# Kernel optimization log

Hardware: AMD Instinct MI355X
Metric: run time of the kernel (lower is better)

Reference implementation:

```python
import jax, jax.numpy as jnp
import numpy as np

N_AGENTS, RNN_H, N_HEADS, GAT_D, EMB, SDIM = 16, 64, 4, 32, 32, 128


def setup_inputs() -> dict:
    key = jax.random.key(0)
    ks = jax.random.split(key, 16)
    xav = lambda k, shp: jax.random.normal(k, shp, jnp.float32) * (2.0 / sum(shp)) ** 0.5
    return {
        'agent_qs': jax.random.normal(ks[0], (32, 128, N_AGENTS), jnp.float32),
        'states': jax.random.normal(ks[1], (32, 128, SDIM), jnp.float32),
        'hidden_states': jax.random.normal(ks[2], (32, 128, N_AGENTS, RNN_H), jnp.float32),
        'uncertainty': jax.random.uniform(ks[3], (32, 128, 1), jnp.float32),
        'W_gat': xav(ks[4], (RNN_H, N_HEADS * GAT_D)) * 1.414,
        'att_a': xav(ks[5], (1, N_HEADS, 2 * GAT_D)) * 1.414,
        'w1s_W': xav(ks[6], (SDIM + 1, N_HEADS * EMB * GAT_D)),
        'w1s_b': jnp.zeros((N_HEADS * EMB * GAT_D,), jnp.float32),
        'b1_W': xav(ks[7], (SDIM, EMB)),
        'b1_b': jnp.zeros((EMB,), jnp.float32),
        'wf_W': xav(ks[8], (SDIM, EMB)),
        'wf_b': jnp.zeros((EMB,), jnp.float32),
        'V1_W': xav(ks[9], (SDIM, EMB)),
        'V1_b': jnp.zeros((EMB,), jnp.float32),
        'V2_W': xav(ks[10], (EMB, 1)),
        'V2_b': jnp.zeros((1,), jnp.float32),
    }


def gat(h, W_gat, att_a):
    B, n, _ = h.shape
    hp = (h @ W_gat).reshape(B, n, N_HEADS, GAT_D).transpose(0, 2, 1, 3)  # (B,H,n,d)
    a_src, a_dst = att_a[0, :, :GAT_D], att_a[0, :, GAT_D:]  # (H,d) each
    # e[b,h,i,j] = <hp_i, a_src> + <hp_j, a_dst>  (same math as concat+dot)
    src = jnp.einsum('bhnd,hd->bhn', hp, a_src)
    dst = jnp.einsum('bhnd,hd->bhn', hp, a_dst)
    e = jax.nn.leaky_relu(src[:, :, :, None] + dst[:, :, None, :], 0.2)
    attn = jax.nn.softmax(e, axis=-1)
    return jax.nn.elu(jnp.einsum('bhij,bhjd->bhid', attn, hp))  # (B,H,n,d)


def reference(agent_qs, states, hidden_states, uncertainty, W_gat, att_a,
              w1s_W, w1s_b, b1_W, b1_b, wf_W, wf_b, V1_W, V1_b, V2_W, V2_b):
    bs = agent_qs.shape[0]
    s = states.reshape(-1, SDIM)                      # (B,S)
    qs = agent_qs.reshape(-1, 1, N_AGENTS)            # (B,1,n)
    hs = hidden_states.reshape(-1, N_AGENTS, RNN_H)   # (B,n,R)
    unc = uncertainty.reshape(-1, 1)
    s_aug = jnp.concatenate([s, unc], axis=1)         # (B,S+1)

    g = gat(hs, W_gat, att_a)                         # (B,H,n,d)

    w1_state = (s_aug @ w1s_W + w1s_b).reshape(-1, N_HEADS, EMB, GAT_D)
    w1_heads = jnp.abs(jnp.einsum('bhed,bhnd->bhen', w1_state, g))  # (B,H,E,n)
    w1 = w1_heads.mean(axis=1).transpose(0, 2, 1)     # (B,n,E)

    b1 = (s @ b1_W + b1_b)[:, None, :]                # (B,1,E)
    hidden = jax.nn.elu(jnp.einsum('bin,bne->bie', qs, w1) + b1)  # (B,1,E)

    w_final = jnp.abs(s @ wf_W + wf_b)[:, :, None]    # (B,E,1)
    v = (jax.nn.relu(s @ V1_W + V1_b) @ V2_W + V2_b)[:, None, :]  # (B,1,1)
    y = jnp.einsum('bie,bej->bij', hidden, w_final) + v
    return y.reshape(bs, -1, 1)
```

## Files before the change

### kernel.cpp

```cpp
#include <hip/hip_runtime.h>
#include <hip/hip_bf16.h>
#include <math.h>


typedef __attribute__((ext_vector_type(8))) short short8;
typedef __attribute__((ext_vector_type(8))) unsigned short ushort8;
typedef __attribute__((ext_vector_type(4))) float float4v;
typedef __attribute__((ext_vector_type(4))) _Float16 half4v;

static __device__ inline unsigned short f2bf(float f) {
    unsigned int x;
    __builtin_memcpy(&x, &f, 4);
    unsigned int r = x + 0x7fffu + ((x >> 16) & 1u);
    return (unsigned short)(r >> 16);
}

static __device__ inline unsigned int cvtpk(float lo, float hi) {
    __hip_bfloat162 h = __float22bfloat162_rn(make_float2(lo, hi));
    unsigned int u;
    __builtin_memcpy(&u, &h, 4);
    return u;
}

static __device__ inline short8 pack8(float4 f0, float4 f1) {
    unsigned int u[4] = {cvtpk(f0.x, f0.y), cvtpk(f0.z, f0.w),
                         cvtpk(f1.x, f1.y), cvtpk(f1.z, f1.w)};
    short8 s;
    __builtin_memcpy(&s, u, 16);
    return s;
}

__global__ __launch_bounds__(256) void k0_prep(
    const float* __restrict__ w1s_W,
    const float* __restrict__ W_gat,
    const float* __restrict__ att_a,
    const float* __restrict__ states,
    const float* __restrict__ b1_W, const float* __restrict__ b1_b,
    const float* __restrict__ wf_W, const float* __restrict__ wf_b,
    const float* __restrict__ V1_W, const float* __restrict__ V1_b,
    const float* __restrict__ V2_W, const float* __restrict__ V2_b,
    unsigned short* __restrict__ w1sTf,
    unsigned short* __restrict__ WgTf,
    unsigned short* __restrict__ Sbf,
    float* __restrict__ b1v, float* __restrict__ wfv,
    float* __restrict__ out)
{
    __shared__ __align__(16) char SMEM[26112];
    const int tid = threadIdx.x, bx = blockIdx.x;

    if (bx < 256) {
        unsigned short* T = (unsigned short*)SMEM;
        const int c0 = bx * 16;
        const int cc = tid & 15, kr = tid >> 4;
        #pragma unroll
        for (int t = 0; t < 8; ++t) {
            int k = t * 16 + kr;
            T[cc * 136 + k] = f2bf(w1s_W[(size_t)k * 4096 + c0 + cc]);
        }
        __syncthreads();
        const int ks = tid >> 6, q = (tid >> 4) & 3, mm = tid & 15;
        *(ushort8*)&w1sTf[(size_t)bx * 2048 + tid * 8] =
            *(const ushort8*)&T[mm * 136 + ks * 32 + q * 8];
    } else if (bx == 256) {
        unsigned short* T = (unsigned short*)SMEM;
        #pragma unroll
        for (int t = 0; t < 32; ++t) {
            int i = t * 256 + tid;
            int k = i >> 7, c = i & 127;
            T[c * 72 + k] = f2bf(W_gat[k * 128 + c]);
        }
        __syncthreads();
        #pragma unroll
        for (int t = 0; t < 4; ++t) {
            int i = t * 256 + tid;
            int nt = i >> 7, w = i & 127;
            int kh = w >> 6, q = (w >> 4) & 3, mm = w & 15;
            *(ushort8*)&WgTf[nt * 1024 + w * 8] =
                *(const ushort8*)&T[(nt * 16 + mm) * 72 + kh * 32 + q * 8];
        }
        {
            const int k = tid >> 2, h = tid & 3;
            float ss = 0.f, dd = 0.f;
            #pragma unroll
            for (int d = 0; d < 32; ++d) {
                float wv = W_gat[k * 128 + h * 32 + d];
                ss = fmaf(wv, att_a[h * 64 + d], ss);
                dd = fmaf(wv, att_a[h * 64 + 32 + d], dd);
            }
            const int base = 8192 + (k >> 5) * 512 + ((k >> 3) & 3) * 128 + (k & 7);
            WgTf[base + h * 8]       = f2bf(ss);
            WgTf[base + (4 + h) * 8] = f2bf(dd);
        }
        #pragma unroll
        for (int t = 0; t < 2; ++t) {
            int i = t * 256 + tid;
            int kh = i >> 8, q = (i >> 6) & 3, mm = 8 + ((i >> 3) & 7), j = i & 7;
            WgTf[8192 + kh * 512 + q * 128 + mm * 8 + j] = 0;
        }
    } else {
        unsigned short* WLu = (unsigned short*)SMEM;
        for (int i = tid; i < 12288; i += 256) {
            float v = (i < 4096) ? b1_W[i] : (i < 8192 ? wf_W[i - 4096] : V1_W[i - 8192]);
            int set = i >> 12, k = (i >> 5) & 127, e = i & 31;
            WLu[set * 4352 + k * 34 + e] = f2bf(v);
        }
        __syncthreads();

        const int wave = tid >> 6, lane = tid & 63, mm = lane & 15, q = lane >> 4;
        const int b0w = (bx - 257) * 64 + wave * 16;

        short8 a[4];
        #pragma unroll
        for (int ks = 0; ks < 4; ++ks) {
            const float* sp = states + (size_t)(b0w + mm) * 128 + ks * 32 + q * 8;
            a[ks] = pack8(*(const float4*)sp, *(const float4*)(sp + 4));
        }
        #pragma unroll
        for (int ks = 0; ks < 4; ++ks)
            *(short8*)&Sbf[(size_t)(b0w + mm) * 128 + ks * 32 + q * 8] = a[ks];

        float4v accT[6];
        #pragma unroll
        for (int nt = 0; nt < 6; ++nt) accT[nt] = (float4v){0.f, 0.f, 0.f, 0.f};
        #pragma unroll
        for (int nt = 0; nt < 6; ++nt) {
            const int set = nt >> 1, e = (nt & 1) * 16 + mm;
            #pragma unroll
            for (int ks = 0; ks < 4; ++ks) {
                ushort8 bfu;
                #pragma unroll
                for (int j = 0; j < 8; ++j)
                    bfu[j] = WLu[set * 4352 + (ks * 32 + q * 8 + j) * 34 + e];
                short8 bf;
                __builtin_memcpy(&bf, &bfu, 16);
                accT[nt] = __builtin_amdgcn_mfma_f32_16x16x32_bf16(a[ks], bf, accT[nt], 0, 0, 0);
            }
        }
        float vsum[4] = {0.f, 0.f, 0.f, 0.f};
        #pragma unroll
        for (int p = 0; p < 2; ++p) {
            const int e = p * 16 + mm;
            const float bb1 = b1_b[e], bwf = wf_b[e], bv1 = V1_b[e], v2 = V2_W[e];
            #pragma unroll
            for (int reg = 0; reg < 4; ++reg) {
                const int row = b0w + q * 4 + reg;
                b1v[(size_t)row * 32 + e] = accT[p][reg] + bb1;
                wfv[(size_t)row * 32 + e] = fabsf(accT[2 + p][reg] + bwf);
                vsum[reg] += fmaxf(accT[4 + p][reg] + bv1, 0.f) * v2;
            }
        }
        #pragma unroll
        for (int reg = 0; reg < 4; ++reg) {
            vsum[reg] += __shfl_xor(vsum[reg], 1);
            vsum[reg] += __shfl_xor(vsum[reg], 2);
            vsum[reg] += __shfl_xor(vsum[reg], 4);
            vsum[reg] += __shfl_xor(vsum[reg], 8);
        }
        if (mm == 0) {
            #pragma unroll
            for (int reg = 0; reg < 4; ++reg)
                out[b0w + q * 4 + reg] = vsum[reg] + V2_b[0];
        }
    }
}

__global__ __launch_bounds__(256) void k2a_gemm(
    const unsigned short* __restrict__ w1sTf,
    const unsigned short* __restrict__ Sbf,
    const float* __restrict__ uncertainty,
    const float* __restrict__ w1s_W,
    const float* __restrict__ w1s_b,
    unsigned short* __restrict__ W2)
{
    const int bx = blockIdx.x;
    const int rb = bx >> 4, pg = bx & 15;
    const int wave = threadIdx.x >> 6, lane = threadIdx.x & 63;
    const int m = lane & 15, quad = lane >> 4;
    const int ep = pg * 4 + wave;
    const int ct0 = ep * 4;

    const float* w128 = w1s_W + (size_t)128 * 4096;

    short8 A[4][4];
    #pragma unroll
    for (int t = 0; t < 4; ++t)
        #pragma unroll
        for (int ks = 0; ks < 4; ++ks)
            A[t][ks] = *(const short8*)&w1sTf[(size_t)(ct0 + t) * 2048 + ks * 512 + lane * 8];

    float wf[4][4], bb[4][4];
    #pragma unroll
    for (int t = 0; t < 4; ++t) {
        float4 w4 = *(const float4*)&w128[(ct0 + t) * 16 + quad * 4];
        float4 b4 = *(const float4*)&w1s_b[(ct0 + t) * 16 + quad * 4];
        wf[t][0] = w4.x; wf[t][1] = w4.y; wf[t][2] = w4.z; wf[t][3] = w4.w;
        bb[t][0] = b4.x; bb[t][1] = b4.y; bb[t][2] = b4.z; bb[t][3] = b4.w;
    }

    #pragma unroll
    for (int c = 0; c < 4; ++c) {
        const int r0c = rb * 64 + c * 16;
        const float us = uncertainty[r0c + m];
        short8 Bf[4];
        #pragma unroll
        for (int ks = 0; ks < 4; ++ks)
            Bf[ks] = *(const short8*)&Sbf[(size_t)(r0c + m) * 128 + ks * 32 + quad * 8];

        float4v z[4];
        #pragma unroll
        for (int t = 0; t < 4; ++t) z[t] = (float4v){0.f, 0.f, 0.f, 0.f};
        #pragma unroll
        for (int t = 0; t < 4; ++t)
            #pragma unroll
            for (int ks = 0; ks < 4; ++ks)
                z[t] = __builtin_amdgcn_mfma_f32_16x16x32_bf16(A[t][ks], Bf[ks], z[t], 0, 0, 0);

        #pragma unroll
        for (int half = 0; half < 2; ++half) {
            const int tA = half * 2, tB = half * 2 + 1;
            unsigned int wpk[4];
            #pragma unroll
            for (int reg = 0; reg < 4; ++reg) {
                float za = z[tA][reg] + us * wf[tA][reg] + bb[tA][reg];
                float zb = z[tB][reg] + us * wf[tB][reg] + bb[tB][reg];
                wpk[reg] = cvtpk(za, zb);
            }
            short8 pk;
            __builtin_memcpy(&pk, wpk, 16);
            const int E = ep * 2 + half;
            const int eo = (E >> 4) * 512 + (E & 15) * 32 + quad * 8;
            *(short8*)&W2[(size_t)(r0c + m) * 4096 + eo] = pk;
        }
    }
}

__global__ __launch_bounds__(256) void k1_gatmix(
    const float* __restrict__ hidden_states,
    const unsigned short* __restrict__ WgTf,
    const unsigned short* __restrict__ W2,
    const float* __restrict__ agent_qs,
    const float* __restrict__ b1v, const float* __restrict__ wfv,
    float* __restrict__ out)
{
    const int wave = threadIdx.x >> 6;
    const int b = blockIdx.x * 4 + wave;
    const int lane = threadIdx.x & 63, m = lane & 15, quad = lane >> 4;
    __shared__ __align__(16) float sc[4 * 320];
    float* scr = &sc[wave * 320];

    short8 wfr[8];
    #pragma unroll
    for (int i = 0; i < 8; ++i)
        wfr[i] = *(const short8*)&W2[(size_t)b * 4096 + i * 512 + m * 32 + quad * 8];
    const float qs_m = agent_qs[b * 16 + m];

    const float* hrow = hidden_states + ((size_t)b * 16 + m) * 64;
    float4 f0 = *(const float4*)(hrow + quad * 8);
    float4 f1 = *(const float4*)(hrow + quad * 8 + 4);
    short8 a0 = pack8(f0, f1);
    f0 = *(const float4*)(hrow + 32 + quad * 8);
    f1 = *(const float4*)(hrow + 32 + quad * 8 + 4);
    short8 a1 = pack8(f0, f1);

    float4v hpt[9];
    #pragma unroll
    for (int nt = 0; nt < 9; ++nt) {
        short8 bf0 = *(const short8*)&WgTf[nt * 1024 + lane * 8];
        short8 bf1 = *(const short8*)&WgTf[nt * 1024 + 512 + lane * 8];
        float4v z = (float4v){0.f, 0.f, 0.f, 0.f};
        z = __builtin_amdgcn_mfma_f32_16x16x32_bf16(a0, bf0, z, 0, 0, 0);
        z = __builtin_amdgcn_mfma_f32_16x16x32_bf16(a1, bf1, z, 0, 0, 0);
        hpt[nt] = z;
    }

    {
        float4 pr = {hpt[8][0], hpt[8][1], hpt[8][2], hpt[8][3]};
        *(float4*)&scr[m * 20 + quad * 4] = pr;
    }

    float Sacc[2][4] = {};

    #pragma unroll
    for (int h = 0; h < 4; ++h) {
        const float src_m = scr[h * 20 + m];
        float4 pdv = *(const float4*)&scr[(4 + h) * 20 + quad * 4];
        float pd[4] = {pdv.x, pdv.y, pdv.z, pdv.w};

        float e_[4];
        #pragma unroll
        for (int jj = 0; jj < 4; ++jj) {
            float x = src_m + pd[jj];
            e_[jj] = fmaxf(x, 0.2f * x);
        }
        float mx = fmaxf(fmaxf(e_[0], e_[1]), fmaxf(e_[2], e_[3]));
        mx = fmaxf(mx, __shfl_xor(mx, 16));
        mx = fmaxf(mx, __shfl_xor(mx, 32));
        float p_[4], ssum = 0.f;
        #pragma unroll
        for (int jj = 0; jj < 4; ++jj) { p_[jj] = __expf(e_[jj] - mx); ssum += p_[jj]; }
        ssum += __shfl_xor(ssum, 16);
        ssum += __shfl_xor(ssum, 32);
        const float inv = __builtin_amdgcn_rcpf(ssum);

        half4v bfrag;
        #pragma unroll
        for (int jj = 0; jj < 4; ++jj) bfrag[jj] = (_Float16)(p_[jj] * inv);

        float4v zp[2];
        #pragma unroll
        for (int p = 0; p < 2; ++p) {
            float4v ct = hpt[2 * h + p];
            half4v afrag;
            #pragma unroll
            for (int t = 0; t < 4; ++t) afrag[t] = (_Float16)ct[t];
            float4v z = (float4v){0.f, 0.f, 0.f, 0.f};
            zp[p] = __builtin_amdgcn_mfma_f32_16x16x16f16(afrag, bfrag, z, 0, 0, 0);
        }
        unsigned int w[4];
        #pragma unroll
        for (int t = 0; t < 4; ++t) {
            float x0 = zp[0][t];
            x0 = (x0 > 0.f) ? x0 : (__expf(x0) - 1.f);
            float x1 = zp[1][t];
            x1 = (x1 > 0.f) ? x1 : (__expf(x1) - 1.f);
            w[t] = cvtpk(x0, x1);
        }
        short8 gfrag;
        __builtin_memcpy(&gfrag, w, 16);

        #pragma unroll
        for (int H = 0; H < 2; ++H) {
            float4v z = (float4v){0.f, 0.f, 0.f, 0.f};
            z = __builtin_amdgcn_mfma_f32_16x16x32_bf16(wfr[h * 2 + H], gfrag, z, 0, 0, 0);
            #pragma unroll
            for (int reg = 0; reg < 4; ++reg)
                Sacc[H][reg] += fabsf(z[reg]);
        }
    }

    float local = 0.f;
    #pragma unroll
    for (int H = 0; H < 2; ++H) {
        float sn[4];
        #pragma unroll
        for (int reg = 0; reg < 4; ++reg) sn[reg] = Sacc[H][reg] * qs_m;
        #pragma unroll
        for (int mask = 1; mask <= 8; mask <<= 1) {
            #pragma unroll
            for (int reg = 0; reg < 4; ++reg) sn[reg] += __shfl_xor(sn[reg], mask);
        }
        float4 b4 = *(const float4*)&b1v[(size_t)b * 32 + H * 16 + quad * 4];
        float4 w4 = *(const float4*)&wfv[(size_t)b * 32 + H * 16 + quad * 4];
        float bq[4] = {b4.x, b4.y, b4.z, b4.w};
        float wq[4] = {w4.x, w4.y, w4.z, w4.w};
        #pragma unroll
        for (int reg = 0; reg < 4; ++reg) {
            float hid = 0.25f * sn[reg] + bq[reg];
            hid = (hid > 0.f) ? hid : expm1f(hid);
            local = fmaf(hid, wq[reg], local);
        }
    }
    local += __shfl_xor(local, 16);
    local += __shfl_xor(local, 32);
    if (lane == 0) out[b] = out[b] + local;
}

extern "C" void kernel_launch(void* const* d_in, const int* in_sizes, int n_in,
                              void* d_out, int out_size, void* d_ws, size_t ws_size,
                              hipStream_t stream)
{
    const float* agent_qs      = (const float*)d_in[0];
    const float* states        = (const float*)d_in[1];
    const float* hidden_states = (const float*)d_in[2];
    const float* uncertainty   = (const float*)d_in[3];
    const float* W_gat         = (const float*)d_in[4];
    const float* att_a         = (const float*)d_in[5];
    const float* w1s_W         = (const float*)d_in[6];
    const float* w1s_b         = (const float*)d_in[7];
    const float* b1_W          = (const float*)d_in[8];
    const float* b1_b          = (const float*)d_in[9];
    const float* wf_W          = (const float*)d_in[10];
    const float* wf_b          = (const float*)d_in[11];
    const float* V1_W          = (const float*)d_in[12];
    const float* V1_b          = (const float*)d_in[13];
    const float* V2_W          = (const float*)d_in[14];
    const float* V2_b          = (const float*)d_in[15];

    char* w = (char*)d_ws;
    unsigned short* w1sTf   = (unsigned short*)w;  w += (size_t)524288 * 2;
    unsigned short* WgTf    = (unsigned short*)w;  w += (size_t)9216 * 2;
    unsigned short* Sbf     = (unsigned short*)w;  w += (size_t)524288 * 2;
    unsigned short* W2      = (unsigned short*)w;  w += (size_t)16777216 * 2;
    float* b1v              = (float*)w;           w += (size_t)131072 * 4;
    float* wfv              = (float*)w;           w += (size_t)131072 * 4;
    float* out              = (float*)d_out;

    k0_prep<<<321, 256, 0, stream>>>(w1s_W, W_gat, att_a, states,
                                     b1_W, b1_b, wf_W, wf_b, V1_W, V1_b,
                                     V2_W, V2_b, w1sTf, WgTf, Sbf, b1v, wfv, out);

    k2a_gemm<<<1024, 256, 0, stream>>>(w1sTf, Sbf, uncertainty, w1s_W, w1s_b, W2);

    k1_gatmix<<<1024, 256, 0, stream>>>(hidden_states, WgTf, W2, agent_qs,
                                        b1v, wfv, out);
}
```

Before: 130.3 us.

## Split GAT-mix work per head across waves and halve GEMM tile per wave

The GAT mixing kernel now assigns one batch element per block, with each of the four waves handling one attention head, and combines head results through shared memory after a block barrier. The W2 GEMM kernel gives each wave one embedding pair instead of two, doubling its grid. The aim is more parallelism and fewer live registers per wave, which should raise occupancy. In exchange, each block of the mixing kernel recomputes the shared projection tile and adds a __syncthreads plus shared-memory reduction, and both kernels now launch more blocks.

```diff
diff --git a/kernel.cpp b/kernel.cpp
--- a/kernel.cpp
+++ b/kernel.cpp
@@ -173,30 +173,32 @@
     unsigned short* __restrict__ W2)
 {
     const int bx = blockIdx.x;
-    const int rb = bx >> 4, pg = bx & 15;
+    const int rb = bx >> 5, pg = bx & 31;
     const int wave = threadIdx.x >> 6, lane = threadIdx.x & 63;
     const int m = lane & 15, quad = lane >> 4;
-    const int ep = pg * 4 + wave;
-    const int ct0 = ep * 4;
+    const int E = pg * 4 + wave;
+    const int ct0 = E * 2;
 
     const float* w128 = w1s_W + (size_t)128 * 4096;
 
-    short8 A[4][4];
-    #pragma unroll
-    for (int t = 0; t < 4; ++t)
+    short8 A[2][4];
+    #pragma unroll
+    for (int t = 0; t < 2; ++t)
         #pragma unroll
         for (int ks = 0; ks < 4; ++ks)
             A[t][ks] = *(const short8*)&w1sTf[(size_t)(ct0 + t) * 2048 + ks * 512 + lane * 8];
 
-    float wf[4][4], bb[4][4];
-    #pragma unroll
-    for (int t = 0; t < 4; ++t) {
+    float wf[2][4], bb[2][4];
+    #pragma unroll
+    for (int t = 0; t < 2; ++t) {
         float4 w4 = *(const float4*)&w128[(ct0 + t) * 16 + quad * 4];
         float4 b4 = *(const float4*)&w1s_b[(ct0 + t) * 16 + quad * 4];
         wf[t][0] = w4.x; wf[t][1] = w4.y; wf[t][2] = w4.z; wf[t][3] = w4.w;
         bb[t][0] = b4.x; bb[t][1] = b4.y; bb[t][2] = b4.z; bb[t][3] = b4.w;
     }
 
+    const int eo = (E >> 4) * 512 + (E & 15) * 32 + quad * 8;
+
     #pragma unroll
     for (int c = 0; c < 4; ++c) {
         const int r0c = rb * 64 + c * 16;
@@ -206,31 +208,23 @@
         for (int ks = 0; ks < 4; ++ks)
             Bf[ks] = *(const short8*)&Sbf[(size_t)(r0c + m) * 128 + ks * 32 + quad * 8];
 
-        float4v z[4];
-        #pragma unroll
-        for (int t = 0; t < 4; ++t) z[t] = (float4v){0.f, 0.f, 0.f, 0.f};
-        #pragma unroll
-        for (int t = 0; t < 4; ++t)
-            #pragma unroll
-            for (int ks = 0; ks < 4; ++ks)
-                z[t] = __builtin_amdgcn_mfma_f32_16x16x32_bf16(A[t][ks], Bf[ks], z[t], 0, 0, 0);
-
-        #pragma unroll
-        for (int half = 0; half < 2; ++half) {
-            const int tA = half * 2, tB = half * 2 + 1;
-            unsigned int wpk[4];
-            #pragma unroll
-            for (int reg = 0; reg < 4; ++reg) {
-                float za = z[tA][reg] + us * wf[tA][reg] + bb[tA][reg];
-                float zb = z[tB][reg] + us * wf[tB][reg] + bb[tB][reg];
-                wpk[reg] = cvtpk(za, zb);
-            }
-            short8 pk;
-            __builtin_memcpy(&pk, wpk, 16);
-            const int E = ep * 2 + half;
-            const int eo = (E >> 4) * 512 + (E & 15) * 32 + quad * 8;
-            *(short8*)&W2[(size_t)(r0c + m) * 4096 + eo] = pk;
-        }
+        float4v z0 = (float4v){0.f, 0.f, 0.f, 0.f};
+        float4v z1 = (float4v){0.f, 0.f, 0.f, 0.f};
+        #pragma unroll
+        for (int ks = 0; ks < 4; ++ks) {
+            z0 = __builtin_amdgcn_mfma_f32_16x16x32_bf16(A[0][ks], Bf[ks], z0, 0, 0, 0);
+            z1 = __builtin_amdgcn_mfma_f32_16x16x32_bf16(A[1][ks], Bf[ks], z1, 0, 0, 0);
+        }
+        unsigned int wpk[4];
+        #pragma unroll
+        for (int reg = 0; reg < 4; ++reg) {
+            float za = z0[reg] + us * wf[0][reg] + bb[0][reg];
+            float zb = z1[reg] + us * wf[1][reg] + bb[1][reg];
+            wpk[reg] = cvtpk(za, zb);
+        }
+        short8 pk;
+        __builtin_memcpy(&pk, wpk, 16);
+        *(short8*)&W2[(size_t)(r0c + m) * 4096 + eo] = pk;
     }
 }
 
@@ -242,16 +236,17 @@
     const float* __restrict__ b1v, const float* __restrict__ wfv,
     float* __restrict__ out)
 {
-    const int wave = threadIdx.x >> 6;
-    const int b = blockIdx.x * 4 + wave;
+    const int h = threadIdx.x >> 6;
+    const int b = blockIdx.x;
     const int lane = threadIdx.x & 63, m = lane & 15, quad = lane >> 4;
     __shared__ __align__(16) float sc[4 * 320];
-    float* scr = &sc[wave * 320];
-
-    short8 wfr[8];
-    #pragma unroll
-    for (int i = 0; i < 8; ++i)
-        wfr[i] = *(const short8*)&W2[(size_t)b * 4096 + i * 512 + m * 32 + quad * 8];
+    __shared__ float red[128];
+    float* scr = &sc[h * 320];
+
+    short8 wfr[2];
+    #pragma unroll
+    for (int H = 0; H < 2; ++H)
+        wfr[H] = *(const short8*)&W2[(size_t)b * 4096 + (h * 2 + H) * 512 + m * 32 + quad * 8];
     const float qs_m = agent_qs[b * 16 + m];
 
     const float* hrow = hidden_states + ((size_t)b * 16 + m) * 64;
@@ -262,107 +257,110 @@
     f1 = *(const float4*)(hrow + 32 + quad * 8 + 4);
     short8 a1 = pack8(f0, f1);
 
-    float4v hpt[9];
-    #pragma unroll
-    for (int nt = 0; nt < 9; ++nt) {
+    float4v hpt[2], prj;
+    #pragma unroll
+    for (int p = 0; p < 2; ++p) {
+        const int nt = 2 * h + p;
         short8 bf0 = *(const short8*)&WgTf[nt * 1024 + lane * 8];
         short8 bf1 = *(const short8*)&WgTf[nt * 1024 + 512 + lane * 8];
         float4v z = (float4v){0.f, 0.f, 0.f, 0.f};
         z = __builtin_amdgcn_mfma_f32_16x16x32_bf16(a0, bf0, z, 0, 0, 0);
         z = __builtin_amdgcn_mfma_f32_16x16x32_bf16(a1, bf1, z, 0, 0, 0);
-        hpt[nt] = z;
-    }
-
+        hpt[p] = z;
+    }
     {
-        float4 pr = {hpt[8][0], hpt[8][1], hpt[8][2], hpt[8][3]};
+        short8 bf0 = *(const short8*)&WgTf[8 * 1024 + lane * 8];
+        short8 bf1 = *(const short8*)&WgTf[8 * 1024 + 512 + lane * 8];
+        float4v z = (float4v){0.f, 0.f, 0.f, 0.f};
+        z = __builtin_amdgcn_mfma_f32_16x16x32_bf16(a0, bf0, z, 0, 0, 0);
+        z = __builtin_amdgcn_mfma_f32_16x16x32_bf16(a1, bf1, z, 0, 0, 0);
+        prj = z;
+    }
+
+    {
+        float4 pr = {prj[0], prj[1], prj[2], prj[3]};
         *(float4*)&scr[m * 20 + quad * 4] = pr;
     }
 
-    float Sacc[2][4] = {};
-
-    #pragma unroll
-    for (int h = 0; h < 4; ++h) {
-        const float src_m = scr[h * 20 + m];
-        float4 pdv = *(const float4*)&scr[(4 + h) * 20 + quad * 4];
-        float pd[4] = {pdv.x, pdv.y, pdv.z, pdv.w};
-
-        float e_[4];
-        #pragma unroll
-        for (int jj = 0; jj < 4; ++jj) {
-            float x = src_m + pd[jj];
-            e_[jj] = fmaxf(x, 0.2f * x);
-        }
-        float mx = fmaxf(fmaxf(e_[0], e_[1]), fmaxf(e_[2], e_[3]));
-        mx = fmaxf(mx, __shfl_xor(mx, 16));
-        mx = fmaxf(mx, __shfl_xor(mx, 32));
-        float p_[4], ssum = 0.f;
-        #pragma unroll
-        for (int jj = 0; jj < 4; ++jj) { p_[jj] = __expf(e_[jj] - mx); ssum += p_[jj]; }
-        ssum += __shfl_xor(ssum, 16);
-        ssum += __shfl_xor(ssum, 32);
-        const float inv = __builtin_amdgcn_rcpf(ssum);
-
-        half4v bfrag;
-        #pragma unroll
-        for (int jj = 0; jj < 4; ++jj) bfrag[jj] = (_Float16)(p_[jj] * inv);
-
-        float4v zp[2];
-        #pragma unroll
-        for (int p = 0; p < 2; ++p) {
-            float4v ct = hpt[2 * h + p];
-            half4v afrag;
-            #pragma unroll
-            for (int t = 0; t < 4; ++t) afrag[t] = (_Float16)ct[t];
-            float4v z = (float4v){0.f, 0.f, 0.f, 0.f};
-            zp[p] = __builtin_amdgcn_mfma_f32_16x16x16f16(afrag, bfrag, z, 0, 0, 0);
-        }
-        unsigned int w[4];
-        #pragma unroll
-        for (int t = 0; t < 4; ++t) {
-            float x0 = zp[0][t];
-            x0 = (x0 > 0.f) ? x0 : (__expf(x0) - 1.f);
-            float x1 = zp[1][t];
-            x1 = (x1 > 0.f) ? x1 : (__expf(x1) - 1.f);
-            w[t] = cvtpk(x0, x1);
-        }
-        short8 gfrag;
-        __builtin_memcpy(&gfrag, w, 16);
-
-        #pragma unroll
-        for (int H = 0; H < 2; ++H) {
-            float4v z = (float4v){0.f, 0.f, 0.f, 0.f};
-            z = __builtin_amdgcn_mfma_f32_16x16x32_bf16(wfr[h * 2 + H], gfrag, z, 0, 0, 0);
+    const float src_m = scr[h * 20 + m];
+    float4 pdv = *(const float4*)&scr[(4 + h) * 20 + quad * 4];
+    float pd[4] = {pdv.x, pdv.y, pdv.z, pdv.w};
+
+    float e_[4];
+    #pragma unroll
+    for (int jj = 0; jj < 4; ++jj) {
+        float x = src_m + pd[jj];
+        e_[jj] = fmaxf(x, 0.2f * x);
+    }
+    float mx = fmaxf(fmaxf(e_[0], e_[1]), fmaxf(e_[2], e_[3]));
+    mx = fmaxf(mx, __shfl_xor(mx, 16));
+    mx = fmaxf(mx, __shfl_xor(mx, 32));
+    float p_[4], ssum = 0.f;
+    #pragma unroll
+    for (int jj = 0; jj < 4; ++jj) { p_[jj] = __expf(e_[jj] - mx); ssum += p_[jj]; }
+    ssum += __shfl_xor(ssum, 16);
+    ssum += __shfl_xor(ssum, 32);
+    const float inv = __builtin_amdgcn_rcpf(ssum);
+
+    half4v bfrag;
+    #pragma unroll
+    for (int jj = 0; jj < 4; ++jj) bfrag[jj] = (_Float16)(p_[jj] * inv);
+
+    float4v zp[2];
+    #pragma unroll
+    for (int p = 0; p < 2; ++p) {
+        float4v ct = hpt[p];
+        half4v afrag;
+        #pragma unroll
+        for (int t = 0; t < 4; ++t) afrag[t] = (_Float16)ct[t];
+        float4v z = (float4v){0.f, 0.f, 0.f, 0.f};
+        zp[p] = __builtin_amdgcn_mfma_f32_16x16x16f16(afrag, bfrag, z, 0, 0, 0);
+    }
+    unsigned int w[4];
+    #pragma unroll
+    for (int t = 0; t < 4; ++t) {
+        float x0 = zp[0][t];
+        x0 = (x0 > 0.f) ? x0 : (__expf(x0) - 1.f);
+        float x1 = zp[1][t];
+        x1 = (x1 > 0.f) ? x1 : (__expf(x1) - 1.f);
+        w[t] = cvtpk(x0, x1);
+    }
+    short8 gfrag;
+    __builtin_memcpy(&gfrag, w, 16);
+
+    #pragma unroll
+    for (int H = 0; H < 2; ++H) {
+        float4v z = (float4v){0.f, 0.f, 0.f, 0.f};
+        z = __builtin_amdgcn_mfma_f32_16x16x32_bf16(wfr[H], gfrag, z, 0, 0, 0);
+        float sn[4];
+        #pragma unroll
+        for (int reg = 0; reg < 4; ++reg) sn[reg] = fabsf(z[reg]) * qs_m;
+        #pragma unroll
+        for (int mask = 1; mask <= 8; mask <<= 1) {
+            #pragma unroll
+            for (int reg = 0; reg < 4; ++reg) sn[reg] += __shfl_xor(sn[reg], mask);
+        }
+        if (m == 0) {
             #pragma unroll
             for (int reg = 0; reg < 4; ++reg)
-                Sacc[H][reg] += fabsf(z[reg]);
-        }
-    }
-
-    float local = 0.f;
-    #pragma unroll
-    for (int H = 0; H < 2; ++H) {
-        float sn[4];
-        #pragma unroll
-        for (int reg = 0; reg < 4; ++reg) sn[reg] = Sacc[H][reg] * qs_m;
-        #pragma unroll
-        for (int mask = 1; mask <= 8; mask <<= 1) {
-            #pragma unroll
-            for (int reg = 0; reg < 4; ++reg) sn[reg] += __shfl_xor(sn[reg], mask);
-        }
-        float4 b4 = *(const float4*)&b1v[(size_t)b * 32 + H * 16 + quad * 4];
-        float4 w4 = *(const float4*)&wfv[(size_t)b * 32 + H * 16 + quad * 4];
-        float bq[4] = {b4.x, b4.y, b4.z, b4.w};
-        float wq[4] = {w4.x, w4.y, w4.z, w4.w};
-        #pragma unroll
-        for (int reg = 0; reg < 4; ++reg) {
-            float hid = 0.25f * sn[reg] + bq[reg];
-            hid = (hid > 0.f) ? hid : expm1f(hid);
-            local = fmaf(hid, wq[reg], local);
-        }
-    }
-    local += __shfl_xor(local, 16);
-    local += __shfl_xor(local, 32);
-    if (lane == 0) out[b] = out[b] + local;
+                red[h * 32 + H * 16 + quad * 4 + reg] = sn[reg];
+        }
+    }
+    __syncthreads();
+
+    if (h == 0) {
+        const int e = lane & 31;
+        float s4 = red[e] + red[32 + e] + red[64 + e] + red[96 + e];
+        float hid = 0.25f * s4 + b1v[(size_t)b * 32 + e];
+        hid = (hid > 0.f) ? hid : expm1f(hid);
+        float local = hid * wfv[(size_t)b * 32 + e];
+        local += __shfl_xor(local, 1);
+        local += __shfl_xor(local, 2);
+        local += __shfl_xor(local, 4);
+        local += __shfl_xor(local, 8);
+        local += __shfl_xor(local, 16);
+        if (lane == 0) out[b] = out[b] + local;
+    }
 }
 
 extern "C" void kernel_launch(void* const* d_in, const int* in_sizes, int n_in,
@@ -399,8 +397,8 @@
                                      b1_W, b1_b, wf_W, wf_b, V1_W, V1_b,
                                      V2_W, V2_b, w1sTf, WgTf, Sbf, b1v, wfv, out);
 
-    k2a_gemm<<<1024, 256, 0, stream>>>(w1sTf, Sbf, uncertainty, w1s_W, w1s_b, W2);
-
-    k1_gatmix<<<1024, 256, 0, stream>>>(hidden_states, WgTf, W2, agent_qs,
+    k2a_gemm<<<2048, 256, 0, stream>>>(w1sTf, Sbf, uncertainty, w1s_W, w1s_b, W2);
+
+    k1_gatmix<<<4096, 256, 0, stream>>>(hidden_states, WgTf, W2, agent_qs,
                                         b1v, wfv, out);
 }
```

New measurement: 139.6 us. 1.07x slower.

## Fuse prep and hypernet GEMM into one kernel, converting weights on the fly

Applied to the files above, without the earlier changes.

Merges the prep kernel and the w1s GEMM kernel into a single launch. Each GEMM block now reads the fp32 w1s_W and states directly and converts them to bf16 in registers, so the pre-transposed bf16 copies and the extra launch are gone. The small linear layers read weights straight from global memory instead of staging them through shared memory. In exchange, each block does strided uncoalesced fp32 reads of w1s_W (stride 4096). It also halves per-wave column tiles, doubling the grid to 2048 GEMM blocks with redundant weight conversion.

```diff
diff --git a/kernel.cpp b/kernel.cpp
--- a/kernel.cpp
+++ b/kernel.cpp
@@ -30,39 +30,83 @@
     return s;
 }
 
-__global__ __launch_bounds__(256) void k0_prep(
+__global__ __launch_bounds__(256) void kA_fused(
     const float* __restrict__ w1s_W,
     const float* __restrict__ W_gat,
     const float* __restrict__ att_a,
     const float* __restrict__ states,
+    const float* __restrict__ uncertainty,
+    const float* __restrict__ w1s_b,
     const float* __restrict__ b1_W, const float* __restrict__ b1_b,
     const float* __restrict__ wf_W, const float* __restrict__ wf_b,
     const float* __restrict__ V1_W, const float* __restrict__ V1_b,
     const float* __restrict__ V2_W, const float* __restrict__ V2_b,
-    unsigned short* __restrict__ w1sTf,
     unsigned short* __restrict__ WgTf,
-    unsigned short* __restrict__ Sbf,
+    unsigned short* __restrict__ W2,
     float* __restrict__ b1v, float* __restrict__ wfv,
     float* __restrict__ out)
 {
-    __shared__ __align__(16) char SMEM[26112];
+    __shared__ __align__(16) unsigned short T[128 * 72];
     const int tid = threadIdx.x, bx = blockIdx.x;
-
-    if (bx < 256) {
-        unsigned short* T = (unsigned short*)SMEM;
-        const int c0 = bx * 16;
-        const int cc = tid & 15, kr = tid >> 4;
-        #pragma unroll
-        for (int t = 0; t < 8; ++t) {
-            int k = t * 16 + kr;
-            T[cc * 136 + k] = f2bf(w1s_W[(size_t)k * 4096 + c0 + cc]);
-        }
-        __syncthreads();
-        const int ks = tid >> 6, q = (tid >> 4) & 3, mm = tid & 15;
-        *(ushort8*)&w1sTf[(size_t)bx * 2048 + tid * 8] =
-            *(const ushort8*)&T[mm * 136 + ks * 32 + q * 8];
-    } else if (bx == 256) {
-        unsigned short* T = (unsigned short*)SMEM;
+    const int wave = tid >> 6, lane = tid & 63;
+    const int m = lane & 15, quad = lane >> 4;
+
+    if (bx < 64) {
+        const int b0w = bx * 64 + wave * 16;
+
+        short8 a[4];
+        #pragma unroll
+        for (int ks = 0; ks < 4; ++ks) {
+            const float* sp = states + (size_t)(b0w + m) * 128 + ks * 32 + quad * 8;
+            a[ks] = pack8(*(const float4*)sp, *(const float4*)(sp + 4));
+        }
+        float4v accT[6];
+        #pragma unroll
+        for (int nt = 0; nt < 6; ++nt) accT[nt] = (float4v){0.f, 0.f, 0.f, 0.f};
+        #pragma unroll
+        for (int nt = 0; nt < 6; ++nt) {
+            const float* Wset = (nt < 2) ? b1_W : (nt < 4 ? wf_W : V1_W);
+            const int e = (nt & 1) * 16 + m;
+            #pragma unroll
+            for (int ks = 0; ks < 4; ++ks) {
+                unsigned int u[4];
+                #pragma unroll
+                for (int jp = 0; jp < 4; ++jp) {
+                    float g0 = Wset[(ks * 32 + quad * 8 + 2 * jp) * 32 + e];
+                    float g1 = Wset[(ks * 32 + quad * 8 + 2 * jp + 1) * 32 + e];
+                    u[jp] = cvtpk(g0, g1);
+                }
+                short8 bf;
+                __builtin_memcpy(&bf, u, 16);
+                accT[nt] = __builtin_amdgcn_mfma_f32_16x16x32_bf16(a[ks], bf, accT[nt], 0, 0, 0);
+            }
+        }
+        float vsum[4] = {0.f, 0.f, 0.f, 0.f};
+        #pragma unroll
+        for (int p = 0; p < 2; ++p) {
+            const int e = p * 16 + m;
+            const float bb1 = b1_b[e], bwf = wf_b[e], bv1 = V1_b[e], v2 = V2_W[e];
+            #pragma unroll
+            for (int reg = 0; reg < 4; ++reg) {
+                const int row = b0w + quad * 4 + reg;
+                b1v[(size_t)row * 32 + e] = accT[p][reg] + bb1;
+                wfv[(size_t)row * 32 + e] = fabsf(accT[2 + p][reg] + bwf);
+                vsum[reg] += fmaxf(accT[4 + p][reg] + bv1, 0.f) * v2;
+            }
+        }
+        #pragma unroll
+        for (int reg = 0; reg < 4; ++reg) {
+            vsum[reg] += __shfl_xor(vsum[reg], 1);
+            vsum[reg] += __shfl_xor(vsum[reg], 2);
+            vsum[reg] += __shfl_xor(vsum[reg], 4);
+            vsum[reg] += __shfl_xor(vsum[reg], 8);
+        }
+        if (m == 0) {
+            #pragma unroll
+            for (int reg = 0; reg < 4; ++reg)
+                out[b0w + quad * 4 + reg] = vsum[reg] + V2_b[0];
+        }
+    } else if (bx == 64) {
         #pragma unroll
         for (int t = 0; t < 32; ++t) {
             int i = t * 256 + tid;
@@ -94,141 +138,72 @@
         #pragma unroll
         for (int t = 0; t < 2; ++t) {
             int i = t * 256 + tid;
-            int kh = i >> 8, q = (i >> 6) & 3, mm = 8 + ((i >> 3) & 7), j = i & 7;
-            WgTf[8192 + kh * 512 + q * 128 + mm * 8 + j] = 0;
+            int kh = i >> 8, q2 = (i >> 6) & 3, mm = 8 + ((i >> 3) & 7), j = i & 7;
+            WgTf[8192 + kh * 512 + q2 * 128 + mm * 8 + j] = 0;
         }
     } else {
-        unsigned short* WLu = (unsigned short*)SMEM;
-        for (int i = tid; i < 12288; i += 256) {
-            float v = (i < 4096) ? b1_W[i] : (i < 8192 ? wf_W[i - 4096] : V1_W[i - 8192]);
-            int set = i >> 12, k = (i >> 5) & 127, e = i & 31;
-            WLu[set * 4352 + k * 34 + e] = f2bf(v);
-        }
-        __syncthreads();
-
-        const int wave = tid >> 6, lane = tid & 63, mm = lane & 15, q = lane >> 4;
-        const int b0w = (bx - 257) * 64 + wave * 16;
-
-        short8 a[4];
-        #pragma unroll
-        for (int ks = 0; ks < 4; ++ks) {
-            const float* sp = states + (size_t)(b0w + mm) * 128 + ks * 32 + q * 8;
-            a[ks] = pack8(*(const float4*)sp, *(const float4*)(sp + 4));
-        }
-        #pragma unroll
-        for (int ks = 0; ks < 4; ++ks)
-            *(short8*)&Sbf[(size_t)(b0w + mm) * 128 + ks * 32 + q * 8] = a[ks];
-
-        float4v accT[6];
-        #pragma unroll
-        for (int nt = 0; nt < 6; ++nt) accT[nt] = (float4v){0.f, 0.f, 0.f, 0.f};
-        #pragma unroll
-        for (int nt = 0; nt < 6; ++nt) {
-            const int set = nt >> 1, e = (nt & 1) * 16 + mm;
+        const int gb = bx - 65;
+        const int rb = gb >> 5, pg = gb & 31;
+        const int E = pg * 4 + wave;
+        const int ct0 = E * 2;
+
+        const float* w128 = w1s_W + (size_t)128 * 4096;
+
+        short8 A[2][4];
+        #pragma unroll
+        for (int t = 0; t < 2; ++t) {
+            const int col = (ct0 + t) * 16 + m;
             #pragma unroll
             for (int ks = 0; ks < 4; ++ks) {
-                ushort8 bfu;
+                unsigned int u[4];
                 #pragma unroll
-                for (int j = 0; j < 8; ++j)
-                    bfu[j] = WLu[set * 4352 + (ks * 32 + q * 8 + j) * 34 + e];
-                short8 bf;
-                __builtin_memcpy(&bf, &bfu, 16);
-                accT[nt] = __builtin_amdgcn_mfma_f32_16x16x32_bf16(a[ks], bf, accT[nt], 0, 0, 0);
-            }
-        }
-        float vsum[4] = {0.f, 0.f, 0.f, 0.f};
-        #pragma unroll
-        for (int p = 0; p < 2; ++p) {
-            const int e = p * 16 + mm;
-            const float bb1 = b1_b[e], bwf = wf_b[e], bv1 = V1_b[e], v2 = V2_W[e];
+                for (int jp = 0; jp < 4; ++jp) {
+                    float g0 = w1s_W[(size_t)(ks * 32 + quad * 8 + 2 * jp) * 4096 + col];
+                    float g1 = w1s_W[(size_t)(ks * 32 + quad * 8 + 2 * jp + 1) * 4096 + col];
+                    u[jp] = cvtpk(g0, g1);
+                }
+                __builtin_memcpy(&A[t][ks], u, 16);
+            }
+        }
+
+        float wf[2][4], bb[2][4];
+        #pragma unroll
+        for (int t = 0; t < 2; ++t) {
+            float4 w4 = *(const float4*)&w128[(ct0 + t) * 16 + quad * 4];
+            float4 b4 = *(const float4*)&w1s_b[(ct0 + t) * 16 + quad * 4];
+            wf[t][0] = w4.x; wf[t][1] = w4.y; wf[t][2] = w4.z; wf[t][3] = w4.w;
+            bb[t][0] = b4.x; bb[t][1] = b4.y; bb[t][2] = b4.z; bb[t][3] = b4.w;
+        }
+
+        const int eo = (E >> 4) * 512 + (E & 15) * 32 + quad * 8;
+
+        #pragma unroll
+        for (int c = 0; c < 4; ++c) {
+            const int r0c = rb * 64 + c * 16;
+            const float us = uncertainty[r0c + m];
+            short8 Bf[4];
+            #pragma unroll
+            for (int ks = 0; ks < 4; ++ks) {
+                const float* sp = states + (size_t)(r0c + m) * 128 + ks * 32 + quad * 8;
+                Bf[ks] = pack8(*(const float4*)sp, *(const float4*)(sp + 4));
+            }
+
+            float4v z0 = (float4v){0.f, 0.f, 0.f, 0.f};
+            float4v z1 = (float4v){0.f, 0.f, 0.f, 0.f};
+            #pragma unroll
+            for (int ks = 0; ks < 4; ++ks) {
+                z0 = __builtin_amdgcn_mfma_f32_16x16x32_bf16(A[0][ks], Bf[ks], z0, 0, 0, 0);
+                z1 = __builtin_amdgcn_mfma_f32_16x16x32_bf16(A[1][ks], Bf[ks], z1, 0, 0, 0);
+            }
+            unsigned int wpk[4];
             #pragma unroll
             for (int reg = 0; reg < 4; ++reg) {
-                const int row = b0w + q * 4 + reg;
-                b1v[(size_t)row * 32 + e] = accT[p][reg] + bb1;
-                wfv[(size_t)row * 32 + e] = fabsf(accT[2 + p][reg] + bwf);
-                vsum[reg] += fmaxf(accT[4 + p][reg] + bv1, 0.f) * v2;
-            }
-        }
-        #pragma unroll
-        for (int reg = 0; reg < 4; ++reg) {
-            vsum[reg] += __shfl_xor(vsum[reg], 1);
-            vsum[reg] += __shfl_xor(vsum[reg], 2);
-            vsum[reg] += __shfl_xor(vsum[reg], 4);
-            vsum[reg] += __shfl_xor(vsum[reg], 8);
-        }
-        if (mm == 0) {
-            #pragma unroll
-            for (int reg = 0; reg < 4; ++reg)
-                out[b0w + q * 4 + reg] = vsum[reg] + V2_b[0];
-        }
-    }
-}
-
-__global__ __launch_bounds__(256) void k2a_gemm(
-    const unsigned short* __restrict__ w1sTf,
-    const unsigned short* __restrict__ Sbf,
-    const float* __restrict__ uncertainty,
-    const float* __restrict__ w1s_W,
-    const float* __restrict__ w1s_b,
-    unsigned short* __restrict__ W2)
-{
-    const int bx = blockIdx.x;
-    const int rb = bx >> 4, pg = bx & 15;
-    const int wave = threadIdx.x >> 6, lane = threadIdx.x & 63;
-    const int m = lane & 15, quad = lane >> 4;
-    const int ep = pg * 4 + wave;
-    const int ct0 = ep * 4;
-
-    const float* w128 = w1s_W + (size_t)128 * 4096;
-
-    short8 A[4][4];
-    #pragma unroll
-    for (int t = 0; t < 4; ++t)
-        #pragma unroll
-        for (int ks = 0; ks < 4; ++ks)
-            A[t][ks] = *(const short8*)&w1sTf[(size_t)(ct0 + t) * 2048 + ks * 512 + lane * 8];
-
-    float wf[4][4], bb[4][4];
-    #pragma unroll
-    for (int t = 0; t < 4; ++t) {
-        float4 w4 = *(const float4*)&w128[(ct0 + t) * 16 + quad * 4];
-        float4 b4 = *(const float4*)&w1s_b[(ct0 + t) * 16 + quad * 4];
-        wf[t][0] = w4.x; wf[t][1] = w4.y; wf[t][2] = w4.z; wf[t][3] = w4.w;
-        bb[t][0] = b4.x; bb[t][1] = b4.y; bb[t][2] = b4.z; bb[t][3] = b4.w;
-    }
-
-    #pragma unroll
-    for (int c = 0; c < 4; ++c) {
-        const int r0c = rb * 64 + c * 16;
-        const float us = uncertainty[r0c + m];
-        short8 Bf[4];
-        #pragma unroll
-        for (int ks = 0; ks < 4; ++ks)
-            Bf[ks] = *(const short8*)&Sbf[(size_t)(r0c + m) * 128 + ks * 32 + quad * 8];
-
-        float4v z[4];
-        #pragma unroll
-        for (int t = 0; t < 4; ++t) z[t] = (float4v){0.f, 0.f, 0.f, 0.f};
-        #pragma unroll
-        for (int t = 0; t < 4; ++t)
-            #pragma unroll
-            for (int ks = 0; ks < 4; ++ks)
-                z[t] = __builtin_amdgcn_mfma_f32_16x16x32_bf16(A[t][ks], Bf[ks], z[t], 0, 0, 0);
-
-        #pragma unroll
-        for (int half = 0; half < 2; ++half) {
-            const int tA = half * 2, tB = half * 2 + 1;
-            unsigned int wpk[4];
-            #pragma unroll
-            for (int reg = 0; reg < 4; ++reg) {
-                float za = z[tA][reg] + us * wf[tA][reg] + bb[tA][reg];
-                float zb = z[tB][reg] + us * wf[tB][reg] + bb[tB][reg];
+                float za = z0[reg] + us * wf[0][reg] + bb[0][reg];
+                float zb = z1[reg] + us * wf[1][reg] + bb[1][reg];
                 wpk[reg] = cvtpk(za, zb);
             }
             short8 pk;
             __builtin_memcpy(&pk, wpk, 16);
-            const int E = ep * 2 + half;
-            const int eo = (E >> 4) * 512 + (E & 15) * 32 + quad * 8;
             *(short8*)&W2[(size_t)(r0c + m) * 4096 + eo] = pk;
         }
     }
@@ -387,19 +362,16 @@
     const float* V2_b          = (const float*)d_in[15];
 
     char* w = (char*)d_ws;
-    unsigned short* w1sTf   = (unsigned short*)w;  w += (size_t)524288 * 2;
     unsigned short* WgTf    = (unsigned short*)w;  w += (size_t)9216 * 2;
-    unsigned short* Sbf     = (unsigned short*)w;  w += (size_t)524288 * 2;
     unsigned short* W2      = (unsigned short*)w;  w += (size_t)16777216 * 2;
     float* b1v              = (float*)w;           w += (size_t)131072 * 4;
     float* wfv              = (float*)w;           w += (size_t)131072 * 4;
     float* out              = (float*)d_out;
 
-    k0_prep<<<321, 256, 0, stream>>>(w1s_W, W_gat, att_a, states,
-                                     b1_W, b1_b, wf_W, wf_b, V1_W, V1_b,
-                                     V2_W, V2_b, w1sTf, WgTf, Sbf, b1v, wfv, out);
-
-    k2a_gemm<<<1024, 256, 0, stream>>>(w1sTf, Sbf, uncertainty, w1s_W, w1s_b, W2);
+    kA_fused<<<2113, 256, 0, stream>>>(w1s_W, W_gat, att_a, states, uncertainty,
+                                       w1s_b, b1_W, b1_b, wf_W, wf_b,
+                                       V1_W, V1_b, V2_W, V2_b,
+                                       WgTf, W2, b1v, wfv, out);
 
     k1_gatmix<<<1024, 256, 0, stream>>>(hidden_states, WgTf, W2, agent_qs,
                                         b1v, wfv, out);
```

Measured after the change: 143.1 us. 1.1x slower.
